# Performance work log

Measured on AMD Instinct MI355X. Metric: run time of the kernel, lower is better.

The kernel has to match this reference:

```python
import jax, jax.numpy as jnp
import numpy as np

EPS = 1e-5  # clamp floor in BitNet activation quantization


def _bitnet_act_quant(x):
    # Match transformers.integrations.bitnet.ActQuant: per-last-dim int8 fake-quant.
    scale = 127.0 / jnp.clip(jnp.max(jnp.abs(x), axis=-1, keepdims=True), EPS)
    return jnp.clip(jnp.round(x * scale), -128.0, 127.0) / scale


def setup_inputs() -> dict:
    key = jax.random.key(0)
    k1, k2, k3, k4 = jax.random.split(key, 4)
    B, S, D, O = 1, 4096, 4096, 4096  # batch, seq_len, in_features, out_features
    x = jax.random.normal(k1, (B, S, D), dtype=jnp.float32)
    # Ternary weight matrix in {-1, 0, +1} (what the bit-packed RSR format encodes).
    W = jax.random.randint(k2, (O, D), -1, 2).astype(jnp.float32)
    bias = jax.random.normal(k3, (O,), dtype=jnp.float32) * 0.01
    # BitNet weight_scale (divide mode): positive scalar.
    weight_scale = jax.random.uniform(k4, (), dtype=jnp.float32, minval=0.5, maxval=2.0)
    return {"x": x, "W": W, "bias": bias, "weight_scale": weight_scale}


def reference(x, W, bias, weight_scale):
    # CPU backend path: BitNet activation fake-quant, then ternary GEMV per token.
    q = _bitnet_act_quant(x.astype(jnp.float32))
    out = jnp.einsum('bsd,od->bso', q, W)  # [B, S, O]
    out = out + bias
    out = out / weight_scale  # weight_scale_mode == 'divide'
    return out.astype(x.dtype)
```

## Files before the change

### kernel.cpp

```cpp
#include <hip/hip_runtime.h>
#include <hip/hip_bf16.h>


#define SEQ  4096
#define DIM  4096
#define OUTD 4096

typedef int i32x4 __attribute__((ext_vector_type(4)));
typedef unsigned char u8;

__device__ __forceinline__ void gload16(const void* g, void* lds) {
    __builtin_amdgcn_global_load_lds(
        (const __attribute__((address_space(1))) void*)g,
        (__attribute__((address_space(3))) void*)lds, 16, 0, 0);
}

__device__ __forceinline__ int ldsoff(int r, int kq) {
    const int rp = r >> 1;
    const int w = (((r & 1) << 6) | (kq << 4)) ^ ((rp & 3) << 4);
    return rp * 128 + w;
}

__global__ __launch_bounds__(256) void quant_kernel(
    const float* __restrict__ x, char* __restrict__ q, float* __restrict__ rscale) {
    const int row = blockIdx.x;
    const int t = threadIdx.x;
    const int lane = t & 63, wave = t >> 6;
    const float4* xr = (const float4*)(x + (size_t)row * DIM);

    float4 r[4];
    float m = 0.0f;
#pragma unroll
    for (int i = 0; i < 4; ++i) {
        r[i] = xr[t + 256 * i];
        m = fmaxf(m, fmaxf(fmaxf(fabsf(r[i].x), fabsf(r[i].y)),
                           fmaxf(fabsf(r[i].z), fabsf(r[i].w))));
    }
#pragma unroll
    for (int off = 32; off > 0; off >>= 1)
        m = fmaxf(m, __shfl_xor(m, off, 64));
    __shared__ float red[4];
    if (lane == 0) red[wave] = m;
    __syncthreads();
    const float amax = fmaxf(fmaxf(red[0], red[1]), fmaxf(red[2], red[3]));
    const float scale = 127.0f / fmaxf(amax, 1e-5f);
    if (t == 0) rscale[row] = 1.0f / scale;

    char4* qr = (char4*)(q + (size_t)row * DIM);
#pragma unroll
    for (int i = 0; i < 4; ++i) {
        float q0 = fminf(127.0f, fmaxf(-128.0f, rintf(r[i].x * scale)));
        float q1 = fminf(127.0f, fmaxf(-128.0f, rintf(r[i].y * scale)));
        float q2 = fminf(127.0f, fmaxf(-128.0f, rintf(r[i].z * scale)));
        float q3 = fminf(127.0f, fmaxf(-128.0f, rintf(r[i].w * scale)));
        char4 o;
        o.x = (signed char)q0; o.y = (signed char)q1;
        o.z = (signed char)q2; o.w = (signed char)q3;
        qr[t + 256 * i] = o;
    }
}

__global__ __launch_bounds__(256) void wconv_kernel(
    const float4* __restrict__ W4, char4* __restrict__ Wb4, int n4) {
    int i = blockIdx.x * blockDim.x + threadIdx.x;
    const int stride = gridDim.x * blockDim.x;
    for (; i < n4; i += stride) {
        float4 w = W4[i];
        char4 o;
        o.x = (signed char)w.x; o.y = (signed char)w.y;
        o.z = (signed char)w.z; o.w = (signed char)w.w;
        Wb4[i] = o;
    }
}

__global__ __launch_bounds__(512, 2) void gemm_kernel(
    const u8* __restrict__ A, const u8* __restrict__ B,
    const float* __restrict__ rscale, const float* __restrict__ bias,
    const float* __restrict__ wscale, float* __restrict__ out) {
    __shared__ __align__(16) u8 As[4 * 16384];
    __shared__ __align__(16) u8 Bs[4 * 16384];
    const int tid = threadIdx.x;
    const int lane = tid & 63, wave = tid >> 6;
    const int wr = wave >> 2, wc = wave & 3;
    const int fr = lane & 15, kq = lane >> 4;

    const int bid = blockIdx.x;
    const int swz = (bid & 7) * 32 + (bid >> 3);
    const int brow = swz >> 4, bcol = swz & 15;

    const int v = (tid & 7) ^ ((tid >> 3) & 3);
    const int kb = (v & 3) * 16;
    const int r0 = ((tid >> 3) << 1) + (v >> 2);
    const u8* gA0 = A + (size_t)(brow * 256 + r0) * DIM + kb;
    const u8* gA1 = A + (size_t)(brow * 256 + 128 + r0) * DIM + kb;
    const u8* gB0 = B + (size_t)(bcol * 256 + r0) * DIM + kb;
    const u8* gB1 = B + (size_t)(bcol * 256 + 128 + r0) * DIM + kb;
    u8* lA0 = &As[tid * 16];
    u8* lA1 = &As[8192 + tid * 16];
    u8* lB0 = &Bs[tid * 16];
    u8* lB1 = &Bs[8192 + tid * 16];

#define STAGE(T, S) do { const int _k = (T) * 64;          \
        gload16(gA0 + _k, lA0 + (S) * 16384);              \
        gload16(gA1 + _k, lA1 + (S) * 16384);              \
        gload16(gB0 + _k, lB0 + (S) * 16384);              \
        gload16(gB1 + _k, lB1 + (S) * 16384); } while (0)

    int aoff[8], boff[4];
#pragma unroll
    for (int m = 0; m < 8; ++m) aoff[m] = ldsoff(wr * 128 + m * 16 + fr, kq);
#pragma unroll
    for (int n = 0; n < 4; ++n) boff[n] = ldsoff(wc * 64 + n * 16 + fr, kq);

    i32x4 acc[8][4] = {};

#define COMPUTE(S) do {                                                        \
        i32x4 af[8], bfv[4];                                                   \
        _Pragma("unroll")                                                      \
        for (int n = 0; n < 4; ++n)                                            \
            bfv[n] = *(const i32x4*)&Bs[(S) * 16384 + boff[n]];                \
        _Pragma("unroll")                                                      \
        for (int m = 0; m < 8; ++m)                                            \
            af[m] = *(const i32x4*)&As[(S) * 16384 + aoff[m]];                 \
        _Pragma("unroll")                                                      \
        for (int m = 0; m < 8; ++m)                                            \
            _Pragma("unroll")                                                  \
            for (int n = 0; n < 4; ++n)                                        \
                acc[m][n] = __builtin_amdgcn_mfma_i32_16x16x64_i8(             \
                    af[m], bfv[n], acc[m][n], 0, 0, 0);                        \
    } while (0)

#define VMW(N) asm volatile("s_waitcnt vmcnt(" #N ")" ::: "memory")
#define BAR()  do { asm volatile("" ::: "memory");                             \
                    __builtin_amdgcn_s_barrier();                              \
                    asm volatile("" ::: "memory"); } while (0)

    STAGE(0, 0); STAGE(1, 1); STAGE(2, 2);

    for (int tb = 0; tb < 15; ++tb) {
        const int t = tb * 4;
        VMW(8); BAR(); STAGE(t + 3, 3); COMPUTE(0);
        VMW(8); BAR(); STAGE(t + 4, 0); COMPUTE(1);
        VMW(8); BAR(); STAGE(t + 5, 1); COMPUTE(2);
        VMW(8); BAR(); STAGE(t + 6, 2); COMPUTE(3);
    }
    VMW(8); BAR(); STAGE(63, 3); COMPUTE(0);
    VMW(8); BAR(); COMPUTE(1);
    VMW(4); BAR(); COMPUTE(2);
    VMW(0); BAR(); COMPUTE(3);

    const float invws = 1.0f / wscale[0];
    const int rr0 = brow * 256 + wr * 128 + (kq << 2);
    const int c0 = bcol * 256 + wc * 64 + fr;
    float bv[4];
#pragma unroll
    for (int n = 0; n < 4; ++n) bv[n] = bias[c0 + n * 16] * invws;
#pragma unroll
    for (int m = 0; m < 8; ++m) {
#pragma unroll
        for (int j = 0; j < 4; ++j) {
            const int r = rr0 + m * 16 + j;
            const float rs = rscale[r] * invws;
            float* orow = out + (size_t)r * OUTD + c0;
#pragma unroll
            for (int n = 0; n < 4; ++n)
                orow[n * 16] = (float)acc[m][n][j] * rs + bv[n];
        }
    }
#undef STAGE
#undef COMPUTE
#undef VMW
#undef BAR
}

extern "C" void kernel_launch(void* const* d_in, const int* in_sizes, int n_in,
                              void* d_out, int out_size, void* d_ws, size_t ws_size,
                              hipStream_t stream) {
    const float* x      = (const float*)d_in[0];
    const float* W      = (const float*)d_in[1];
    const float* bias   = (const float*)d_in[2];
    const float* wscale = (const float*)d_in[3];
    float* out = (float*)d_out;

    char* ws = (char*)d_ws;
    char* q_i8 = ws;
    char* w_i8 = ws + (size_t)16777216;
    float* rscale = (float*)(ws + (size_t)33554432);

    quant_kernel<<<SEQ, 256, 0, stream>>>(x, q_i8, rscale);
    wconv_kernel<<<4096, 256, 0, stream>>>((const float4*)W, (char4*)w_i8,
                                           (OUTD * DIM) / 4);
    gemm_kernel<<<256, 512, 0, stream>>>((const u8*)q_i8, (const u8*)w_i8,
                                         rscale, bias, wscale, out);
}
```

Before: 92.88 us.

## Switch GEMM to 32x32x32 int8 MFMA with split-K fragment loads and priority hints

```diff
diff --git a/kernel.cpp b/kernel.cpp
--- a/kernel.cpp
+++ b/kernel.cpp
@@ -7,6 +7,7 @@
 #define OUTD 4096
 
 typedef int i32x4 __attribute__((ext_vector_type(4)));
+typedef int i32x16 __attribute__((ext_vector_type(16)));
 typedef unsigned char u8;
 
 __device__ __forceinline__ void gload16(const void* g, void* lds) {
@@ -82,7 +83,8 @@
     const int tid = threadIdx.x;
     const int lane = tid & 63, wave = tid >> 6;
     const int wr = wave >> 2, wc = wave & 3;
-    const int fr = lane & 15, kq = lane >> 4;
+    const int cl = lane & 31;
+    const int kh = lane >> 5;
 
     const int bid = blockIdx.x;
     const int swz = (bid & 7) * 32 + (bid >> 3);
@@ -106,71 +108,106 @@
         gload16(gB0 + _k, lB0 + (S) * 16384);              \
         gload16(gB1 + _k, lB1 + (S) * 16384); } while (0)
 
-    int aoff[8], boff[4];
-#pragma unroll
-    for (int m = 0; m < 8; ++m) aoff[m] = ldsoff(wr * 128 + m * 16 + fr, kq);
-#pragma unroll
-    for (int n = 0; n < 4; ++n) boff[n] = ldsoff(wc * 64 + n * 16 + fr, kq);
-
-    i32x4 acc[8][4] = {};
-
-#define COMPUTE(S) do {                                                        \
-        i32x4 af[8], bfv[4];                                                   \
+    int aoff[4][2], boff[2][2];
+#pragma unroll
+    for (int m = 0; m < 4; ++m)
+#pragma unroll
+        for (int s = 0; s < 2; ++s)
+            aoff[m][s] = ldsoff(wr * 128 + m * 32 + cl, s * 2 + kh);
+#pragma unroll
+    for (int n = 0; n < 2; ++n)
+#pragma unroll
+        for (int s = 0; s < 2; ++s)
+            boff[n][s] = ldsoff(wc * 64 + n * 32 + cl, s * 2 + kh);
+
+    i32x16 acc[4][2] = {};
+
+#define LOADFRAG(S, s, af, bfv)                                                \
+    _Pragma("unroll")                                                          \
+    for (int m = 0; m < 4; ++m)                                                \
+        af[m] = *(const i32x4*)&As[(S) * 16384 + aoff[m][s]];                  \
+    _Pragma("unroll")                                                          \
+    for (int n = 0; n < 2; ++n)                                                \
+        bfv[n] = *(const i32x4*)&Bs[(S) * 16384 + boff[n][s]];
+
+#define MFMA8(af, bfv)                                                         \
+    __builtin_amdgcn_s_setprio(1);                                             \
+    _Pragma("unroll")                                                          \
+    for (int m = 0; m < 4; ++m)                                                \
         _Pragma("unroll")                                                      \
-        for (int n = 0; n < 4; ++n)                                            \
-            bfv[n] = *(const i32x4*)&Bs[(S) * 16384 + boff[n]];                \
-        _Pragma("unroll")                                                      \
-        for (int m = 0; m < 8; ++m)                                            \
-            af[m] = *(const i32x4*)&As[(S) * 16384 + aoff[m]];                 \
-        _Pragma("unroll")                                                      \
-        for (int m = 0; m < 8; ++m)                                            \
-            _Pragma("unroll")                                                  \
-            for (int n = 0; n < 4; ++n)                                        \
-                acc[m][n] = __builtin_amdgcn_mfma_i32_16x16x64_i8(             \
-                    af[m], bfv[n], acc[m][n], 0, 0, 0);                        \
-    } while (0)
+        for (int n = 0; n < 2; ++n)                                            \
+            acc[m][n] = __builtin_amdgcn_mfma_i32_32x32x32_i8(                 \
+                af[m], bfv[n], acc[m][n], 0, 0, 0);                            \
+    __builtin_amdgcn_s_setprio(0);
 
 #define VMW(N) asm volatile("s_waitcnt vmcnt(" #N ")" ::: "memory")
 #define BAR()  do { asm volatile("" ::: "memory");                             \
                     __builtin_amdgcn_s_barrier();                              \
                     asm volatile("" ::: "memory"); } while (0)
 
+#define TILE_S(S, T) do {                                                      \
+        VMW(8); BAR();                                                         \
+        { i32x4 af[4], bfv[2];                                                 \
+          LOADFRAG(S, 0, af, bfv);                                             \
+          STAGE(T, ((S) + 3) & 3);                                             \
+          MFMA8(af, bfv); }                                                    \
+        { i32x4 af[4], bfv[2];                                                 \
+          LOADFRAG(S, 1, af, bfv);                                             \
+          MFMA8(af, bfv); }                                                    \
+    } while (0)
+
+#define TILE_N(S) do {                                                         \
+        { i32x4 af[4], bfv[2];                                                 \
+          LOADFRAG(S, 0, af, bfv);                                             \
+          MFMA8(af, bfv); }                                                    \
+        { i32x4 af[4], bfv[2];                                                 \
+          LOADFRAG(S, 1, af, bfv);                                             \
+          MFMA8(af, bfv); }                                                    \
+    } while (0)
+
     STAGE(0, 0); STAGE(1, 1); STAGE(2, 2);
 
     for (int tb = 0; tb < 15; ++tb) {
         const int t = tb * 4;
-        VMW(8); BAR(); STAGE(t + 3, 3); COMPUTE(0);
-        VMW(8); BAR(); STAGE(t + 4, 0); COMPUTE(1);
-        VMW(8); BAR(); STAGE(t + 5, 1); COMPUTE(2);
-        VMW(8); BAR(); STAGE(t + 6, 2); COMPUTE(3);
-    }
-    VMW(8); BAR(); STAGE(63, 3); COMPUTE(0);
-    VMW(8); BAR(); COMPUTE(1);
-    VMW(4); BAR(); COMPUTE(2);
-    VMW(0); BAR(); COMPUTE(3);
+        TILE_S(0, t + 3);
+        TILE_S(1, t + 4);
+        TILE_S(2, t + 5);
+        TILE_S(3, t + 6);
+    }
+    TILE_S(0, 63);
+    VMW(8); BAR(); TILE_N(1);
+    VMW(4); BAR(); TILE_N(2);
+    VMW(0); BAR(); TILE_N(3);
 
     const float invws = 1.0f / wscale[0];
-    const int rr0 = brow * 256 + wr * 128 + (kq << 2);
-    const int c0 = bcol * 256 + wc * 64 + fr;
-    float bv[4];
-#pragma unroll
-    for (int n = 0; n < 4; ++n) bv[n] = bias[c0 + n * 16] * invws;
-#pragma unroll
-    for (int m = 0; m < 8; ++m) {
-#pragma unroll
-        for (int j = 0; j < 4; ++j) {
-            const int r = rr0 + m * 16 + j;
-            const float rs = rscale[r] * invws;
-            float* orow = out + (size_t)r * OUTD + c0;
-#pragma unroll
-            for (int n = 0; n < 4; ++n)
-                orow[n * 16] = (float)acc[m][n][j] * rs + bv[n];
+    const int rr0 = brow * 256 + wr * 128 + kh * 4;
+    const int c0 = bcol * 256 + wc * 64 + cl;
+    float bv[2];
+#pragma unroll
+    for (int n = 0; n < 2; ++n) bv[n] = bias[c0 + n * 32] * invws;
+#pragma unroll
+    for (int m = 0; m < 4; ++m) {
+#pragma unroll
+        for (int qg = 0; qg < 4; ++qg) {
+#pragma unroll
+            for (int j = 0; j < 4; ++j) {
+                const int r = rr0 + m * 32 + qg * 8 + j;
+                const int reg = qg * 4 + j;
+                const float rs = rscale[r] * invws;
+                float* orow = out + (size_t)r * OUTD + c0;
+#pragma unroll
+                for (int n = 0; n < 2; ++n)
+                    orow[n * 32] = (float)acc[m][n][reg] * rs + bv[n];
+            }
         }
     }
 #undef STAGE
-#undef COMPUTE
+#undef LOADFRAG
+#undef MFMA8
 #undef VMW
 #undef BAR
+#undef TILE_S
+#undef TILE_N
 }
 
 extern "C" void kernel_launch(void* const* d_in, const int* in_sizes, int n_in,
```

Measured after the change: 101.4 us. 9.2% more time.

## Split MFMA tile into halves, issue LDS reads before staging, add setprio

Applied to the files above, without the earlier changes.

```diff
diff --git a/kernel.cpp b/kernel.cpp
--- a/kernel.cpp
+++ b/kernel.cpp
@@ -114,40 +114,54 @@
 
     i32x4 acc[8][4] = {};
 
-#define COMPUTE(S) do {                                                        \
-        i32x4 af[8], bfv[4];                                                   \
-        _Pragma("unroll")                                                      \
-        for (int n = 0; n < 4; ++n)                                            \
-            bfv[n] = *(const i32x4*)&Bs[(S) * 16384 + boff[n]];                \
-        _Pragma("unroll")                                                      \
-        for (int m = 0; m < 8; ++m)                                            \
-            af[m] = *(const i32x4*)&As[(S) * 16384 + aoff[m]];                 \
-        _Pragma("unroll")                                                      \
-        for (int m = 0; m < 8; ++m)                                            \
-            _Pragma("unroll")                                                  \
-            for (int n = 0; n < 4; ++n)                                        \
-                acc[m][n] = __builtin_amdgcn_mfma_i32_16x16x64_i8(             \
-                    af[m], bfv[n], acc[m][n], 0, 0, 0);                        \
-    } while (0)
-
 #define VMW(N) asm volatile("s_waitcnt vmcnt(" #N ")" ::: "memory")
 #define BAR()  do { asm volatile("" ::: "memory");                             \
                     __builtin_amdgcn_s_barrier();                              \
                     asm volatile("" ::: "memory"); } while (0)
 
+#define TILE_BODY(S, DO_STAGE, T) do {                                         \
+        { i32x4 af[4], bfv[4];                                                 \
+          _Pragma("unroll")                                                    \
+          for (int m = 0; m < 4; ++m)                                          \
+              af[m] = *(const i32x4*)&As[(S) * 16384 + aoff[m]];               \
+          _Pragma("unroll")                                                    \
+          for (int n = 0; n < 4; ++n)                                          \
+              bfv[n] = *(const i32x4*)&Bs[(S) * 16384 + boff[n]];              \
+          if (DO_STAGE) STAGE(T, ((S) + 3) & 3);                               \
+          __builtin_amdgcn_s_setprio(1);                                       \
+          _Pragma("unroll")                                                    \
+          for (int m = 0; m < 4; ++m)                                          \
+              _Pragma("unroll")                                                \
+              for (int n = 0; n < 4; ++n)                                      \
+                  acc[m][n] = __builtin_amdgcn_mfma_i32_16x16x64_i8(           \
+                      af[m], bfv[n], acc[m][n], 0, 0, 0);                      \
+          __builtin_amdgcn_s_setprio(0);                                       \
+          _Pragma("unroll")                                                    \
+          for (int m = 0; m < 4; ++m)                                          \
+              af[m] = *(const i32x4*)&As[(S) * 16384 + aoff[4 + m]];           \
+          __builtin_amdgcn_s_setprio(1);                                       \
+          _Pragma("unroll")                                                    \
+          for (int m = 0; m < 4; ++m)                                          \
+              _Pragma("unroll")                                                \
+              for (int n = 0; n < 4; ++n)                                      \
+                  acc[4 + m][n] = __builtin_amdgcn_mfma_i32_16x16x64_i8(       \
+                      af[m], bfv[n], acc[4 + m][n], 0, 0, 0);                  \
+          __builtin_amdgcn_s_setprio(0); }                                     \
+    } while (0)
+
     STAGE(0, 0); STAGE(1, 1); STAGE(2, 2);
 
     for (int tb = 0; tb < 15; ++tb) {
         const int t = tb * 4;
-        VMW(8); BAR(); STAGE(t + 3, 3); COMPUTE(0);
-        VMW(8); BAR(); STAGE(t + 4, 0); COMPUTE(1);
-        VMW(8); BAR(); STAGE(t + 5, 1); COMPUTE(2);
-        VMW(8); BAR(); STAGE(t + 6, 2); COMPUTE(3);
-    }
-    VMW(8); BAR(); STAGE(63, 3); COMPUTE(0);
-    VMW(8); BAR(); COMPUTE(1);
-    VMW(4); BAR(); COMPUTE(2);
-    VMW(0); BAR(); COMPUTE(3);
+        VMW(8); BAR(); TILE_BODY(0, 1, t + 3);
+        VMW(8); BAR(); TILE_BODY(1, 1, t + 4);
+        VMW(8); BAR(); TILE_BODY(2, 1, t + 5);
+        VMW(8); BAR(); TILE_BODY(3, 1, t + 6);
+    }
+    VMW(8); BAR(); TILE_BODY(0, 1, 63);
+    VMW(8); BAR(); TILE_BODY(1, 0, 0);
+    VMW(4); BAR(); TILE_BODY(2, 0, 0);
+    VMW(0); BAR(); TILE_BODY(3, 0, 0);
 
     const float invws = 1.0f / wscale[0];
     const int rr0 = brow * 256 + wr * 128 + (kq << 2);
@@ -168,9 +182,9 @@
         }
     }
 #undef STAGE
-#undef COMPUTE
 #undef VMW
 #undef BAR
+#undef TILE_BODY
 }
 
 extern "C" void kernel_launch(void* const* d_in, const int* in_sizes, int n_in,
```

After: 95.08 us. 2.4% more time.

## Split GEMM k-tile compute into ping-pong phases with barriers and setprio

Applied to the files above, without the earlier changes.

```diff
diff --git a/kernel.cpp b/kernel.cpp
--- a/kernel.cpp
+++ b/kernel.cpp
@@ -100,54 +100,77 @@
     u8* lB0 = &Bs[tid * 16];
     u8* lB1 = &Bs[8192 + tid * 16];
 
+    int aoff[8], boff[4];
+#pragma unroll
+    for (int m = 0; m < 8; ++m) aoff[m] = ldsoff(wr * 128 + m * 16 + fr, kq);
+#pragma unroll
+    for (int n = 0; n < 4; ++n) boff[n] = ldsoff(wc * 64 + n * 16 + fr, kq);
+
+    i32x4 acc[8][4] = {};
+
+#define VMW(N) asm volatile("s_waitcnt vmcnt(" #N ")" ::: "memory")
+#define BAR()  do { asm volatile("" ::: "memory");                             \
+                    __builtin_amdgcn_s_barrier();                              \
+                    asm volatile("" ::: "memory"); } while (0)
+
+#define PH(S, M0, READB, STMT) do {                                            \
+        if (READB) {                                                           \
+            _Pragma("unroll")                                                  \
+            for (int n = 0; n < 4; ++n)                                        \
+                bfv[n] = *(const i32x4*)&Bs[(S) * 16384 + boff[n]];            \
+        }                                                                      \
+        i32x4 afa = *(const i32x4*)&As[(S) * 16384 + aoff[M0]];                \
+        i32x4 afb = *(const i32x4*)&As[(S) * 16384 + aoff[(M0) + 1]];          \
+        STMT;                                                                  \
+        BAR();                                                                 \
+        __builtin_amdgcn_s_setprio(1);                                         \
+        _Pragma("unroll")                                                      \
+        for (int n = 0; n < 4; ++n)                                            \
+            acc[M0][n] = __builtin_amdgcn_mfma_i32_16x16x64_i8(                \
+                afa, bfv[n], acc[M0][n], 0, 0, 0);                             \
+        _Pragma("unroll")                                                      \
+        for (int n = 0; n < 4; ++n)                                            \
+            acc[(M0) + 1][n] = __builtin_amdgcn_mfma_i32_16x16x64_i8(          \
+                afb, bfv[n], acc[(M0) + 1][n], 0, 0, 0);                       \
+        __builtin_amdgcn_s_setprio(0);                                         \
+        BAR();                                                                 \
+    } while (0)
+
+#define TILE_S(S, T) do {                                                      \
+        i32x4 bfv[4];                                                          \
+        PH(S, 0, 1, gload16(gA0 + (T) * 64, lA0 + (((S) + 3) & 3) * 16384));   \
+        PH(S, 2, 0, gload16(gA1 + (T) * 64, lA1 + (((S) + 3) & 3) * 16384));   \
+        PH(S, 4, 0, gload16(gB0 + (T) * 64, lB0 + (((S) + 3) & 3) * 16384));   \
+        PH(S, 6, 0, gload16(gB1 + (T) * 64, lB1 + (((S) + 3) & 3) * 16384));   \
+    } while (0)
+
+#define TILE_N(S) do {                                                         \
+        i32x4 bfv[4];                                                          \
+        PH(S, 0, 1, (void)0);                                                  \
+        PH(S, 2, 0, (void)0);                                                  \
+        PH(S, 4, 0, (void)0);                                                  \
+        PH(S, 6, 0, (void)0);                                                  \
+    } while (0)
+
 #define STAGE(T, S) do { const int _k = (T) * 64;          \
         gload16(gA0 + _k, lA0 + (S) * 16384);              \
         gload16(gA1 + _k, lA1 + (S) * 16384);              \
         gload16(gB0 + _k, lB0 + (S) * 16384);              \
         gload16(gB1 + _k, lB1 + (S) * 16384); } while (0)
 
-    int aoff[8], boff[4];
-#pragma unroll
-    for (int m = 0; m < 8; ++m) aoff[m] = ldsoff(wr * 128 + m * 16 + fr, kq);
-#pragma unroll
-    for (int n = 0; n < 4; ++n) boff[n] = ldsoff(wc * 64 + n * 16 + fr, kq);
-
-    i32x4 acc[8][4] = {};
-
-#define COMPUTE(S) do {                                                        \
-        i32x4 af[8], bfv[4];                                                   \
-        _Pragma("unroll")                                                      \
-        for (int n = 0; n < 4; ++n)                                            \
-            bfv[n] = *(const i32x4*)&Bs[(S) * 16384 + boff[n]];                \
-        _Pragma("unroll")                                                      \
-        for (int m = 0; m < 8; ++m)                                            \
-            af[m] = *(const i32x4*)&As[(S) * 16384 + aoff[m]];                 \
-        _Pragma("unroll")                                                      \
-        for (int m = 0; m < 8; ++m)                                            \
-            _Pragma("unroll")                                                  \
-            for (int n = 0; n < 4; ++n)                                        \
-                acc[m][n] = __builtin_amdgcn_mfma_i32_16x16x64_i8(             \
-                    af[m], bfv[n], acc[m][n], 0, 0, 0);                        \
-    } while (0)
-
-#define VMW(N) asm volatile("s_waitcnt vmcnt(" #N ")" ::: "memory")
-#define BAR()  do { asm volatile("" ::: "memory");                             \
-                    __builtin_amdgcn_s_barrier();                              \
-                    asm volatile("" ::: "memory"); } while (0)
-
     STAGE(0, 0); STAGE(1, 1); STAGE(2, 2);
 
     for (int tb = 0; tb < 15; ++tb) {
         const int t = tb * 4;
-        VMW(8); BAR(); STAGE(t + 3, 3); COMPUTE(0);
-        VMW(8); BAR(); STAGE(t + 4, 0); COMPUTE(1);
-        VMW(8); BAR(); STAGE(t + 5, 1); COMPUTE(2);
-        VMW(8); BAR(); STAGE(t + 6, 2); COMPUTE(3);
-    }
-    VMW(8); BAR(); STAGE(63, 3); COMPUTE(0);
-    VMW(8); BAR(); COMPUTE(1);
-    VMW(4); BAR(); COMPUTE(2);
-    VMW(0); BAR(); COMPUTE(3);
+        VMW(8); BAR(); TILE_S(0, t + 3);
+        VMW(8); BAR(); TILE_S(1, t + 4);
+        VMW(8); BAR(); TILE_S(2, t + 5);
+        VMW(8); BAR(); TILE_S(3, t + 6);
+    }
+    VMW(8); BAR(); TILE_S(0, 63);
+    VMW(8); BAR(); TILE_N(1);
+    VMW(4); BAR(); TILE_N(2);
+    VMW(0); BAR(); TILE_N(3);
 
     const float invws = 1.0f / wscale[0];
     const int rr0 = brow * 256 + wr * 128 + (kq << 2);
@@ -168,9 +191,11 @@
         }
     }
 #undef STAGE
-#undef COMPUTE
 #undef VMW
 #undef BAR
+#undef PH
+#undef TILE_S
+#undef TILE_N
 }
 
 extern "C" void kernel_launch(void* const* d_in, const int* in_sizes, int n_in,
```

After: 97.19 us. 1.05x slower.
